# Kernel tuning notes

Measured on AMD Instinct MI355X. Metric: run time of the kernel, lower is better.

## Reference

```python
import jax, jax.numpy as jnp
import numpy as np

B, C, HID, H, W = 32, 256, 128, 32, 32  # batch, input_dim, hidden_dim, grid


def conv1x1(x, Wt, b):
    # 1x1 Conv2d == channel-mixing matmul. x: [B,Cin,H,W], Wt: [Cout,Cin]
    return jnp.einsum('oc,bchw->bohw', Wt, x) + b[None, :, None, None]


def setup_inputs() -> dict:
    key = jax.random.key(0)
    ks = jax.random.split(key, 18)
    p = lambda k, shape: (jax.random.normal(k, shape, jnp.float32) * 0.02)
    return {
        'h': jax.random.normal(ks[0], (B, C, H, W), jnp.float32),
        'm': jax.random.normal(ks[1], (B, C, H, W), jnp.float32),
        'Wq': p(ks[2], (HID, C)),  'bq': p(ks[3], (HID,)),
        'Wk': p(ks[4], (HID, C)),  'bk': p(ks[5], (HID,)),
        'Wv': p(ks[6], (C, C)),    'bv': p(ks[7], (C,)),
        'Wk2': p(ks[8], (HID, C)), 'bk2': p(ks[9], (HID,)),
        'Wv2': p(ks[10], (C, C)),  'bv2': p(ks[11], (C,)),
        'Wz': p(ks[12], (2 * C, 2 * C)), 'bz': p(ks[13], (2 * C,)),
        'Wm': p(ks[14], (3 * C, 3 * C)), 'bm': p(ks[15], (3 * C,)),
    }


def reference(h, m, Wq, bq, Wk, bk, Wv, bv, Wk2, bk2, Wv2, bv2, Wz, bz, Wm, bm):
    Bb, Cc, Hh, Ww = h.shape
    HW = Hh * Ww
    # shared query from h: [B, HID, HW]
    q = conv1x1(h, Wq, bq).reshape(Bb, -1, HW)
    # self-attention branch over h (unscaled logits, as in original)
    kh = conv1x1(h, Wk, bk).reshape(Bb, -1, HW)
    A_h = jax.nn.softmax(jnp.einsum('bdp,bdq->bpq', q, kh), axis=-1)  # [B,HW,HW]
    vh = conv1x1(h, Wv, bv).reshape(Bb, Cc, HW)
    Z_h = jnp.einsum('bpq,bcq->bcp', A_h, vh).reshape(Bb, Cc, Hh, Ww)
    # cross-attention branch over memory m with shared q
    km = conv1x1(m, Wk2, bk2).reshape(Bb, -1, HW)
    A_m = jax.nn.softmax(jnp.einsum('bdp,bdq->bpq', q, km), axis=-1)
    vm = conv1x1(m, Wv2, bv2).reshape(Bb, Cc, HW)
    Z_m = jnp.einsum('bpq,bcq->bcp', A_m, vm).reshape(Bb, Cc, Hh, Ww)
    # fuse, then LSTM-style gating
    Z = conv1x1(jnp.concatenate([Z_h, Z_m], axis=1), Wz, bz)          # [B,2C,H,W]
    comb = conv1x1(jnp.concatenate([Z, h], axis=1), Wm, bm)           # [B,3C,H,W]
    mo, mg, mi = jnp.split(comb, 3, axis=1)
    mi = jax.nn.sigmoid(mi)
    new_m = (1.0 - mi) * m + mi * jnp.tanh(mg)
    new_h = jax.nn.sigmoid(mo) * new_m
    return new_h, new_m
```

## Files before the change

### kernel.cpp

```cpp
#include <hip/hip_runtime.h>
#include <hip/hip_bf16.h>

typedef __bf16  v8bf __attribute__((ext_vector_type(8)));
typedef float   v4f  __attribute__((ext_vector_type(4)));
typedef float   f4   __attribute__((ext_vector_type(4)));
typedef unsigned short us8 __attribute__((ext_vector_type(8)));
typedef unsigned short us4 __attribute__((ext_vector_type(4)));
typedef unsigned int u32;

#define BATCH 32
#define CDIM  256
#define HW    1024

#define OFF_HBT 0L
#define OFF_MBT (OFF_HBT + 16777216L)
#define OFF_QKH (OFF_MBT + 16777216L)
#define OFF_QKM (OFF_QKH + 16777216L)
#define OFF_VH  (OFF_QKM + 8388608L)
#define OFF_VM  (OFF_VH  + 16777216L)
#define OFF_ZCT (OFF_VM  + 16777216L)
#define OFF_W   (OFF_ZCT + 33554432L)
#define OFF_B   (OFF_W   + 3866624L)
#define WS_TOTAL (OFF_B + 2944L * 4)
#define W_QK  0
#define W_K2  65536
#define W_V   98304
#define W_V2  163840
#define W_M   491520
#define W_ZT  1081344
#define W_F   1343488
#define B_QK  0
#define B_K2  256
#define B_V   384
#define B_V2  640
#define B_F   2176

__device__ inline unsigned short f2u(float x) {
    __hip_bfloat16 h = __float2bfloat16(x);
    union { __hip_bfloat16 h; unsigned short u; } cv; cv.h = h; return cv.u;
}
__device__ inline float u2f(unsigned short u) {
    union { unsigned short u; __hip_bfloat16 h; } cv; cv.u = u; return __bfloat162float(cv.h);
}
__device__ inline float sigmoidf_(float x) {
    x = fminf(fmaxf(x, -30.f), 30.f);
    return 1.f / (1.f + __expf(-x));
}
__device__ inline float tanhf_(float x) {
    x = fminf(fmaxf(x, -15.f), 15.f);
    float e = __expf(2.f * x);
    return (e - 1.f) / (e + 1.f);
}
__device__ inline void glds16(const unsigned short* g, unsigned short* l) {
    __builtin_amdgcn_global_load_lds(
        (const __attribute__((address_space(1))) u32*)g,
        (__attribute__((address_space(3))) u32*)l, 16, 0, 0);
}

__global__ __launch_bounds__(256)
void prep(const float* __restrict__ hsrc, const float* __restrict__ msrc,
          const float* __restrict__ Wq, const float* __restrict__ Wk,
          const float* __restrict__ Wv, const float* __restrict__ Wk2,
          const float* __restrict__ Wv2, const float* __restrict__ Wz,
          const float* __restrict__ Wm,
          const float* __restrict__ bq, const float* __restrict__ bk,
          const float* __restrict__ bk2, const float* __restrict__ bv,
          const float* __restrict__ bv2, const float* __restrict__ bz,
          const float* __restrict__ bm,
          char* __restrict__ ws)
{
    __shared__ float t[64][68];
    unsigned short* wdst = (unsigned short*)(ws + OFF_W);
    float*          bdst = (float*)(ws + OFF_B);
    const int bid = blockIdx.x;
    const int tid = threadIdx.x;

    if (bid < 6025) {
        const int gid = bid * 256 + tid;
        if (gid < 1081344) {
            const float* s; int off;
            if      (gid <   32768) { s = Wq;  off = gid; }
            else if (gid <   65536) { s = Wk;  off = gid -   32768; }
            else if (gid <   98304) { s = Wk2; off = gid -   65536; }
            else if (gid <  163840) { s = Wv;  off = gid -   98304; }
            else if (gid <  229376) { s = Wv2; off = gid -  163840; }
            else if (gid <  491520) { s = Wz;  off = gid -  229376; }
            else                    { s = Wm;  off = gid -  491520; }
            wdst[gid] = f2u(s[off]);
        } else if (gid < 1343488) {
            const int idx = gid - 1081344;
            const int k = idx >> 9, j = idx & 511;
            wdst[gid] = f2u(Wz[j * 512 + k]);
        } else if (gid < 1540096) {
            const int idx = gid - 1343488;
            const int o = idx >> 8, kk = 512 + (idx & 255);
            wdst[W_F + o * 768 + kk] = f2u(Wm[o * 768 + kk]);
        } else {
            const int bi = gid - 1540096;
            if (bi < 2176) {
                const float* s; int off;
                if      (bi <  128) { s = bq;  off = bi; }
                else if (bi <  256) { s = bk;  off = bi -  128; }
                else if (bi <  384) { s = bk2; off = bi -  256; }
                else if (bi <  640) { s = bv;  off = bi -  384; }
                else if (bi <  896) { s = bv2; off = bi -  640; }
                else if (bi < 1408) { s = bz;  off = bi -  896; }
                else                { s = bm;  off = bi - 1408; }
                bdst[bi] = s[off];
            }
        }
    } else if (bid < 6028) {
        const int o = (bid - 6025) * 256 + tid;
        if (o < 768) {
            float s = bm[o];
            const float* r = Wm + (long)o * 768;
#pragma unroll 8
            for (int j = 0; j < 512; ++j) s += r[j] * bz[j];
            bdst[B_F + o] = s;
        }
    } else {
        const int tz = bid - 6028;
        const int z  = tz >> 6;
        const int p0 = (tz & 15) * 64;
        const int c0 = ((tz >> 4) & 3) * 64;
        const float* src = (z < BATCH) ? hsrc + (long)z * CDIM * HW
                                       : msrc + (long)(z - BATCH) * CDIM * HW;
        unsigned short* dst = (unsigned short*)(ws + ((z < BATCH) ? OFF_HBT : OFF_MBT))
                              + (long)((z < BATCH) ? z : z - BATCH) * HW * CDIM;
        const int r  = tid >> 4;
        const int c4 = (tid & 15) * 4;
#pragma unroll
        for (int i = 0; i < 4; ++i) {
            const f4 v = *reinterpret_cast<const f4*>(src + (long)(c0 + r + 16 * i) * HW + p0 + c4);
            t[r + 16 * i][c4 + 0] = v[0];
            t[r + 16 * i][c4 + 1] = v[1];
            t[r + 16 * i][c4 + 2] = v[2];
            t[r + 16 * i][c4 + 3] = v[3];
        }
        __syncthreads();
#pragma unroll
        for (int i = 0; i < 4; ++i) {
            const int pr = r + 16 * i;
            us4 o;
#pragma unroll
            for (int j = 0; j < 4; ++j) o[j] = f2u(t[c4 + j][pr]);
            *reinterpret_cast<us4*>(dst + (long)(p0 + pr) * CDIM + c0 + c4) = o;
        }
    }
}

__device__ __forceinline__
void gemm_core(const unsigned short* __restrict__ A, int lda,
               const unsigned short* __restrict__ A2, int lda2, int kswitch,
               const unsigned short* __restrict__ Bt, int ldb,
               unsigned short* __restrict__ Cp, int ldc,
               int K, const float* __restrict__ bias, int biasMode,
               int m0, int n0,
               unsigned short* As, unsigned short* Bs)
{
    const int tid  = threadIdx.x;
    const int lane = tid & 63;
    const int w    = tid >> 6;

    v4f acc[4][4];
#pragma unroll
    for (int i = 0; i < 4; ++i)
#pragma unroll
        for (int j = 0; j < 4; ++j) acc[i][j] = v4f{0.f, 0.f, 0.f, 0.f};

    const int wm   = (w >> 1) * 64;
    const int wn   = (w & 1) * 64;
    const int fr   = lane & 15;
    const int g    = lane >> 4;

    const int arow = (w << 3) + (lane >> 3);
    const int acol = (((lane & 7) ^ ((lane >> 3) & 7)) * 8);
    const int lbase = (w << 9);

    for (int k0 = 0; k0 < K; k0 += 64) {
        const unsigned short* Ab; int Al; int Ao;
        if (k0 < kswitch) { Ab = A;  Al = lda;  Ao = k0; }
        else              { Ab = A2; Al = lda2; Ao = k0 - kswitch; }
        const unsigned short* ga = Ab + (long)(m0 + arow) * Al + Ao + acol;
        const unsigned short* gb = Bt + (long)(n0 + arow) * ldb + k0 + acol;
#pragma unroll
        for (int i = 0; i < 4; ++i) {
            glds16(ga + (long)(32 * i) * Al, &As[i * 2048 + lbase]);
            glds16(gb + (long)(32 * i) * ldb, &Bs[i * 2048 + lbase]);
        }
        __syncthreads();
#pragma unroll
        for (int ks = 0; ks < 2; ++ks) {
            const int slot = ((ks * 4 + g) ^ (fr & 7)) * 8;
            v8bf af[4], bfv[4];
#pragma unroll
            for (int mi = 0; mi < 4; ++mi)
                af[mi] = *reinterpret_cast<const v8bf*>(&As[(wm + mi * 16 + fr) * 64 + slot]);
#pragma unroll
            for (int ni = 0; ni < 4; ++ni)
                bfv[ni] = *reinterpret_cast<const v8bf*>(&Bs[(wn + ni * 16 + fr) * 64 + slot]);
#pragma unroll
            for (int mi = 0; mi < 4; ++mi)
#pragma unroll
                for (int ni = 0; ni < 4; ++ni)
                    acc[mi][ni] = __builtin_amdgcn_mfma_f32_16x16x32_bf16(af[mi], bfv[ni], acc[mi][ni], 0, 0, 0);
        }
        __syncthreads();
    }

    const int rbase0 = m0 + wm + g * 4;
#pragma unroll
    for (int mi = 0; mi < 4; ++mi) {
#pragma unroll
        for (int ni = 0; ni < 4; ++ni) {
            const int col = n0 + wn + ni * 16 + fr;
            const int rb  = rbase0 + mi * 16;
            const float bn = (biasMode == 1) ? bias[col] : 0.f;
#pragma unroll
            for (int r = 0; r < 4; ++r) {
                float x = acc[mi][ni][r] + bn;
                if (biasMode == 2) x += bias[rb + r];
                Cp[(long)(rb + r) * ldc + col] = f2u(x);
            }
        }
    }
}

__global__ __launch_bounds__(256)
void gemm_multi(char* __restrict__ ws)
{
    __shared__ unsigned short As[128 * 64];
    __shared__ unsigned short Bs[128 * 64];
    unsigned short* wA = (unsigned short*)(ws + OFF_W);
    float*          bA = (float*)(ws + OFF_B);
    const int id = blockIdx.x;

    if (id < 512) {
        const int b = id >> 4, x = id & 7, y = (id >> 3) & 1;
        const unsigned short* A = (unsigned short*)(ws + OFF_HBT) + (long)b * 262144;
        gemm_core(A, 256, A, 256, 1 << 30, wA + W_QK, 256,
                  (unsigned short*)(ws + OFF_QKH) + (long)b * 262144, 256,
                  256, bA + B_QK, 1, x * 128, y * 128, As, Bs);
    } else if (id < 768) {
        const int idx = id - 512, b = idx >> 3, x = idx & 7;
        const unsigned short* A = (unsigned short*)(ws + OFF_MBT) + (long)b * 262144;
        gemm_core(A, 256, A, 256, 1 << 30, wA + W_K2, 256,
                  (unsigned short*)(ws + OFF_QKM) + (long)b * 131072, 128,
                  256, bA + B_K2, 1, x * 128, 0, As, Bs);
    } else if (id < 1280) {
        const int idx = id - 768, b = idx >> 4, x = idx & 1, y = (idx >> 1) & 7;
        gemm_core(wA + W_V, 256, wA + W_V, 256, 1 << 30,
                  (unsigned short*)(ws + OFF_HBT) + (long)b * 262144, 256,
                  (unsigned short*)(ws + OFF_VH) + (long)b * 262144, 1024,
                  256, bA + B_V, 2, x * 128, y * 128, As, Bs);
    } else if (id < 1792) {
        const int idx = id - 1280, b = idx >> 4, x = idx & 1, y = (idx >> 1) & 7;
        gemm_core(wA + W_V2, 256, wA + W_V2, 256, 1 << 30,
                  (unsigned short*)(ws + OFF_MBT) + (long)b * 262144, 256,
                  (unsigned short*)(ws + OFF_VM) + (long)b * 262144, 1024,
                  256, bA + B_V2, 2, x * 128, y * 128, As, Bs);
    } else {
        const int idx = id - 1792, x = idx % 6, y = idx / 6;
        gemm_core(wA + W_M, 768, wA + W_M, 768, 1 << 30, wA + W_ZT, 512,
                  wA + W_F, 768, 512, bA, 0, x * 128, y * 128, As, Bs);
    }
}

__global__ __launch_bounds__(512, 2)
void comb_gemm(const unsigned short* __restrict__ A, int lda,
               const unsigned short* __restrict__ A2, int lda2, int kswitch,
               const unsigned short* __restrict__ Bt, int ldb,
               int K, const float* __restrict__ bias,
               const float* __restrict__ mIn,
               float* __restrict__ outh, float* __restrict__ outm)
{
    __shared__ unsigned short smem[57344];

    const int nwg = gridDim.x;
    const int wg  = (blockIdx.x & 7) * (nwg >> 3) + (blockIdx.x >> 3);
    const int m0  = (wg >> 2) * 256;
    const int c0  = (wg & 3) * 64;

    const int tid  = threadIdx.x;
    const int lane = tid & 63;
    const int w    = tid >> 6;
    const int fr   = lane & 15;
    const int g    = lane >> 4;
    const int wm   = (w >> 2) * 128;
    const int wn   = (w & 3) * 48;

    const int srow   = tid >> 3;
    const int schunk = ((tid & 7) ^ (srow & 7)) * 8;
    const int sdst   = w * 512;

    v4f acc[8][3];
#pragma unroll
    for (int i = 0; i < 8; ++i)
#pragma unroll
        for (int j = 0; j < 3; ++j) acc[i][j] = v4f{0.f, 0.f, 0.f, 0.f};

    const int nt = K >> 6;

#define STAGE_A(t, bi, i)                                                      \
    { const int k0 = (t) * 64;                                                 \
      const unsigned short* Ab; int Al; int Ao;                                \
      if (k0 < kswitch) { Ab = A;  Al = lda;  Ao = k0; }                       \
      else              { Ab = A2; Al = lda2; Ao = k0 - kswitch; }             \
      glds16(Ab + (long)(m0 + (i) * 64 + srow) * Al + Ao + schunk,             \
             &smem[(bi) * 16384 + (i) * 4096 + sdst]); }
#define STAGE_B(t, bi, i)                                                      \
    { const int k0 = (t) * 64;                                                 \
      glds16(Bt + (long)((i) * 256 + c0 + srow) * ldb + k0 + schunk,           \
             &smem[32768 + (bi) * 12288 + (i) * 4096 + sdst]); }

#pragma unroll
    for (int i = 0; i < 4; ++i) STAGE_A(0, 0, i);
#pragma unroll
    for (int i = 0; i < 3; ++i) STAGE_B(0, 0, i);

    for (int t = 0; t < nt; ++t) {
        __syncthreads();

        const unsigned short* Ar = smem + (t & 1) * 16384;
        const unsigned short* Br = smem + 32768 + (t & 1) * 12288;
        const int nb = (t + 1) & 1;
        const bool more = (t + 1 < nt);

#pragma unroll
        for (int ks = 0; ks < 2; ++ks) {
            v8bf bf[3];
#pragma unroll
            for (int ni = 0; ni < 3; ++ni) {
                const int r = wn + ni * 16 + fr;
                bf[ni] = *reinterpret_cast<const v8bf*>(
                    &Br[r * 64 + ((ks * 4 + g) ^ (r & 7)) * 8]);
            }
#pragma unroll
            for (int hh = 0; hh < 2; ++hh) {
                v8bf af[4];
#pragma unroll
                for (int mi = 0; mi < 4; ++mi) {
                    const int r = wm + (hh * 4 + mi) * 16 + fr;
                    af[mi] = *reinterpret_cast<const v8bf*>(
                        &Ar[r * 64 + ((ks * 4 + g) ^ (r & 7)) * 8]);
                }
                if (more) {
                    const int ph = ks * 2 + hh;
                    if (ph == 0)      { STAGE_A(t + 1, nb, 0); STAGE_A(t + 1, nb, 1); }
                    else if (ph == 1) { STAGE_A(t + 1, nb, 2); STAGE_A(t + 1, nb, 3); }
                    else if (ph == 2) { STAGE_B(t + 1, nb, 0); STAGE_B(t + 1, nb, 1); }
                    else              { STAGE_B(t + 1, nb, 2); }
                }
                __builtin_amdgcn_s_setprio(1);
#pragma unroll
                for (int mi = 0; mi < 4; ++mi)
#pragma unroll
                    for (int ni = 0; ni < 3; ++ni)
                        acc[hh * 4 + mi][ni] = __builtin_amdgcn_mfma_f32_16x16x32_bf16(
                            af[mi], bf[ni], acc[hh * 4 + mi][ni], 0, 0, 0);
                __builtin_amdgcn_s_setprio(0);
            }
        }
    }
#undef STAGE_A
#undef STAGE_B

    __syncthreads();

    unsigned short* Lt = smem;
#pragma unroll
    for (int mi = 0; mi < 8; ++mi) {
#pragma unroll
        for (int ni = 0; ni < 3; ++ni) {
            const int j  = wn + ni * 16 + fr;
            const int cg = ((j >> 6) << 8) + c0 + (j & 63);
            const float bn = bias[cg];
            const int rl = wm + mi * 16 + g * 4;
#pragma unroll
            for (int r = 0; r < 4; ++r)
                Lt[(rl + r) * 194 + j] = f2u(acc[mi][ni][r] + bn);
        }
    }
    __syncthreads();

    const int b     = m0 >> 10;
    const int pbase = m0 & 1023;
    const int pl    = tid & 255;
    const int ch    = tid >> 8;
#pragma unroll 4
    for (int cc = 0; cc < 32; ++cc) {
        const int cl = ch * 32 + cc;
        const float mo  = u2f(Lt[pl * 194 + cl]);
        const float mg  = u2f(Lt[pl * 194 + 64 + cl]);
        const float mi_ = u2f(Lt[pl * 194 + 128 + cl]);
        const long gi = ((long)(b * 256 + c0 + cl)) * 1024 + pbase + pl;
        const float mv = mIn[gi];
        const float ms = sigmoidf_(mi_);
        const float nm = (1.f - ms) * mv + ms * tanhf_(mg);
        const float nh = sigmoidf_(mo) * nm;
        outh[gi] = nh;
        outm[gi] = nm;
    }
}

__global__ __launch_bounds__(512, 4)
void attn_fused(const unsigned short* __restrict__ Qb, long sQ, int ldq,
                const unsigned short* __restrict__ K0, long sK0, int ldk0,
                const unsigned short* __restrict__ V0,
                const unsigned short* __restrict__ K1, long sK1, int ldk1,
                const unsigned short* __restrict__ V1,
                unsigned short* __restrict__ Out, long sO)
{
    __shared__ unsigned short Qs[64 * 128];
    __shared__ unsigned short Ks[64 * 128];
    __shared__ unsigned short Vs[256 * 64];
    __shared__ unsigned short Ps[64 * 64];

    const int id = blockIdx.x;
    const int c8 = id & 7;
    const int k  = id >> 3;
    const int z  = c8 * 8 + (k >> 4);
    const int p0 = (k & 15) * 64;

    const int b  = (z < 32) ? z : z - 32;
    const unsigned short* Kp; const unsigned short* Vp; int ldk, outoff;
    if (z < 32) { Kp = K0 + (long)b * sK0; Vp = V0 + (long)b * 262144L; ldk = ldk0; outoff = 0; }
    else        { Kp = K1 + (long)b * sK1; Vp = V1 + (long)b * 262144L; ldk = ldk1; outoff = 256; }
    const unsigned short* Qp = Qb + (long)b * sQ;
    Out += (long)b * sO;

    const int tid  = threadIdx.x;
    const int lane = tid & 63;
    const int w    = tid >> 6;
    const int fr   = lane & 15;
    const int g    = lane >> 4;
    const int wp   = w >> 2;
    const int wq   = w & 3;

    v4f vacc[2][4];
#pragma unroll
    for (int i = 0; i < 2; ++i)
#pragma unroll
        for (int j = 0; j < 4; ++j) vacc[i][j] = v4f{0.f, 0.f, 0.f, 0.f};
    float rp[2][4];
#pragma unroll
    for (int i = 0; i < 2; ++i)
#pragma unroll
        for (int r = 0; r < 4; ++r) rp[i][r] = 0.f;

    const int srow   = tid >> 4;
    const int schunk = ((tid & 15) ^ (srow & 7)) * 8;
    const int vrow   = tid >> 3;
    const int vchunk = ((tid & 7) ^ (vrow & 7)) * 8;
    const int sdst   = w * 512;
    const int kr     = wq * 16 + fr;

#define STAGE_Q()                                                              \
    { _Pragma("unroll")                                                        \
      for (int i = 0; i < 2; ++i)                                              \
          glds16(Qp + (long)(p0 + i * 32 + srow) * ldq + schunk,               \
                 &Qs[i * 4096 + sdst]); }
#define STAGE_K(t)                                                             \
    { const int kv0 = (t) * 64;                                                \
      _Pragma("unroll")                                                        \
      for (int i = 0; i < 2; ++i)                                              \
          glds16(Kp + (long)(kv0 + i * 32 + srow) * ldk + schunk,              \
                 &Ks[i * 4096 + sdst]); }
#define STAGE_V(t)                                                             \
    { const int kv0 = (t) * 64;                                                \
      _Pragma("unroll")                                                        \
      for (int i = 0; i < 4; ++i)                                              \
          glds16(Vp + (long)(i * 64 + vrow) * 1024 + kv0 + vchunk,             \
                 &Vs[i * 4096 + sdst]); }

    STAGE_Q();
    STAGE_K(0);

    for (int t = 0; t < 16; ++t) {
        __syncthreads();
        STAGE_V(t);

        v4f sacc[2];
#pragma unroll
        for (int mi = 0; mi < 2; ++mi) sacc[mi] = v4f{0.f, 0.f, 0.f, 0.f};
        __builtin_amdgcn_s_setprio(1);
#pragma unroll
        for (int ks = 0; ks < 4; ++ks) {
            const v8bf kf = *reinterpret_cast<const v8bf*>(
                &Ks[kr * 128 + ((ks * 4 + g) ^ (kr & 7)) * 8]);
#pragma unroll
            for (int mi = 0; mi < 2; ++mi) {
                const int qrow = wp * 32 + mi * 16 + fr;
                const v8bf qf = *reinterpret_cast<const v8bf*>(
                    &Qs[qrow * 128 + ((ks * 4 + g) ^ (qrow & 7)) * 8]);
                sacc[mi] = __builtin_amdgcn_mfma_f32_16x16x32_bf16(qf, kf, sacc[mi], 0, 0, 0);
            }
        }
        __builtin_amdgcn_s_setprio(0);
#pragma unroll
        for (int mi = 0; mi < 2; ++mi)
#pragma unroll
            for (int r = 0; r < 4; ++r) {
                const float e = __expf(sacc[mi][r]);
                rp[mi][r] += e;
                const int prow = wp * 32 + mi * 16 + g * 4 + r;
                Ps[prow * 64 + (kr ^ ((prow & 7) << 3))] = f2u(e);
            }

        __syncthreads();
        if (t < 15) STAGE_K(t + 1);

        __builtin_amdgcn_s_setprio(1);
#pragma unroll
        for (int ks = 0; ks < 2; ++ks) {
            v8bf pf[2], vf[4];
#pragma unroll
            for (int mi = 0; mi < 2; ++mi) {
                const int pr = wp * 32 + mi * 16 + fr;
                pf[mi] = *reinterpret_cast<const v8bf*>(
                    &Ps[pr * 64 + ((ks * 4 + g) ^ (pr & 7)) * 8]);
            }
#pragma unroll
            for (int ni = 0; ni < 4; ++ni) {
                const int vr = wq * 64 + ni * 16 + fr;
                vf[ni] = *reinterpret_cast<const v8bf*>(
                    &Vs[vr * 64 + ((ks * 4 + g) ^ (vr & 7)) * 8]);
            }
#pragma unroll
            for (int mi = 0; mi < 2; ++mi)
#pragma unroll
                for (int ni = 0; ni < 4; ++ni)
                    vacc[mi][ni] = __builtin_amdgcn_mfma_f32_16x16x32_bf16(pf[mi], vf[ni], vacc[mi][ni], 0, 0, 0);
        }
        __builtin_amdgcn_s_setprio(0);
    }
#undef STAGE_Q
#undef STAGE_K
#undef STAGE_V

    __syncthreads();
    float* red = reinterpret_cast<float*>(Ps);
#pragma unroll
    for (int mi = 0; mi < 2; ++mi)
#pragma unroll
        for (int r = 0; r < 4; ++r) {
            float v = rp[mi][r];
            v += __shfl_xor(v, 1);
            v += __shfl_xor(v, 2);
            v += __shfl_xor(v, 4);
            v += __shfl_xor(v, 8);
            if (fr == 0) red[wq * 64 + wp * 32 + mi * 16 + g * 4 + r] = v;
        }
    __syncthreads();

#pragma unroll
    for (int mi = 0; mi < 2; ++mi)
#pragma unroll
        for (int r = 0; r < 4; ++r) {
            const int pl = wp * 32 + mi * 16 + g * 4 + r;
            const float inv = 1.f / (red[pl] + red[64 + pl] + red[128 + pl] + red[192 + pl]);
#pragma unroll
            for (int ni = 0; ni < 4; ++ni)
                Out[(long)(p0 + pl) * 512 + outoff + wq * 64 + ni * 16 + fr]
                    = f2u(vacc[mi][ni][r] * inv);
        }
}

extern "C" void kernel_launch(void* const* d_in, const int* in_sizes, int n_in,
                              void* d_out, int out_size, void* d_ws, size_t ws_size,
                              hipStream_t stream)
{
    const float* h   = (const float*)d_in[0];
    const float* m   = (const float*)d_in[1];
    const float* Wq  = (const float*)d_in[2];
    const float* bq  = (const float*)d_in[3];
    const float* Wk  = (const float*)d_in[4];
    const float* bk  = (const float*)d_in[5];
    const float* Wv  = (const float*)d_in[6];
    const float* bv  = (const float*)d_in[7];
    const float* Wk2 = (const float*)d_in[8];
    const float* bk2 = (const float*)d_in[9];
    const float* Wv2 = (const float*)d_in[10];
    const float* bv2 = (const float*)d_in[11];
    const float* Wz  = (const float*)d_in[12];
    const float* bz  = (const float*)d_in[13];
    const float* Wm  = (const float*)d_in[14];
    const float* bm  = (const float*)d_in[15];

    char* ws = (char*)d_ws;
    if (ws_size < (size_t)WS_TOTAL) return;

    unsigned short* hT  = (unsigned short*)(ws + OFF_HBT);
    unsigned short* qkh = (unsigned short*)(ws + OFF_QKH);
    unsigned short* qkm = (unsigned short*)(ws + OFF_QKM);
    unsigned short* vh  = (unsigned short*)(ws + OFF_VH);
    unsigned short* vm  = (unsigned short*)(ws + OFF_VM);
    unsigned short* zct = (unsigned short*)(ws + OFF_ZCT);
    unsigned short* wA  = (unsigned short*)(ws + OFF_W);
    float*          bA  = (float*)(ws + OFF_B);

    float* outh = (float*)d_out;
    float* outm = outh + 8388608L;

    prep<<<dim3(10124), dim3(256), 0, stream>>>(
        h, m, Wq, Wk, Wv, Wk2, Wv2, Wz, Wm,
        bq, bk, bk2, bv, bv2, bz, bm, ws);

    gemm_multi<<<dim3(1816), dim3(256), 0, stream>>>(ws);

    attn_fused<<<dim3(1024), dim3(512), 0, stream>>>(
        qkh, 262144L, 256,
        qkh + 128, 262144L, 256, vh,
        qkm, 131072L, 128, vm,
        zct, 524288L);

    comb_gemm<<<dim3(512), dim3(512), 0, stream>>>(
        zct, 512, hT, 256, 512,
        wA + W_F, 768, 768, bA + B_F, m, outh, outm);
}
```

Baseline: 205.4 us.

## Retile attention to 128 query rows per block with 32-wide KV steps

The fused attention kernel now gives each block 128 query rows instead of 64, so each block covers a full PV output tile per wave (4x4 MFMA accumulators). K/V tiles shrink to 32 keys per iteration, with twice as many iterations. The aim is to halve re-reading of K and V across blocks and raise MFMA work per LDS load. The cost is more accumulator registers, more barriers per unit of work, and only 512 blocks, which may hurt occupancy and load balance.

```diff
diff --git a/kernel.cpp b/kernel.cpp
--- a/kernel.cpp
+++ b/kernel.cpp
@@ -411,16 +411,16 @@
                 const unsigned short* __restrict__ V1,
                 unsigned short* __restrict__ Out, long sO)
 {
-    __shared__ unsigned short Qs[64 * 128];
-    __shared__ unsigned short Ks[64 * 128];
-    __shared__ unsigned short Vs[256 * 64];
-    __shared__ unsigned short Ps[64 * 64];
+    __shared__ unsigned short Qs[128 * 128];
+    __shared__ unsigned short Ks[32 * 128];
+    __shared__ unsigned short Vs[256 * 32];
+    __shared__ unsigned short Ps[128 * 32];
 
     const int id = blockIdx.x;
     const int c8 = id & 7;
     const int k  = id >> 3;
-    const int z  = c8 * 8 + (k >> 4);
-    const int p0 = (k & 15) * 64;
+    const int z  = c8 * 8 + (k >> 3);
+    const int p0 = (k & 7) * 128;
 
     const int b  = (z < 32) ? z : z - 32;
     const unsigned short* Kp; const unsigned short* Vp; int ldk, outoff;
@@ -436,10 +436,14 @@
     const int g    = lane >> 4;
     const int wp   = w >> 2;
     const int wq   = w & 3;
-
-    v4f vacc[2][4];
-#pragma unroll
-    for (int i = 0; i < 2; ++i)
+    const int srow0 = wp * 64 + (wq >> 1) * 32;
+    const int kc0   = (wq & 1) * 16;
+    const int kr    = kc0 + fr;
+    const int wc    = wq * 64;
+
+    v4f vacc[4][4];
+#pragma unroll
+    for (int i = 0; i < 4; ++i)
 #pragma unroll
         for (int j = 0; j < 4; ++j) vacc[i][j] = v4f{0.f, 0.f, 0.f, 0.f};
     float rp[2][4];
@@ -448,35 +452,30 @@
 #pragma unroll
         for (int r = 0; r < 4; ++r) rp[i][r] = 0.f;
 
-    const int srow   = tid >> 4;
-    const int schunk = ((tid & 15) ^ (srow & 7)) * 8;
-    const int vrow   = tid >> 3;
-    const int vchunk = ((tid & 7) ^ (vrow & 7)) * 8;
+    const int qkrow  = tid >> 4;
+    const int qkchk  = ((tid & 15) ^ (qkrow & 7)) * 8;
+    const int vrow   = tid >> 2;
+    const int vchk   = ((tid & 3) ^ (vrow & 3)) * 8;
     const int sdst   = w * 512;
-    const int kr     = wq * 16 + fr;
 
 #define STAGE_Q()                                                              \
     { _Pragma("unroll")                                                        \
-      for (int i = 0; i < 2; ++i)                                              \
-          glds16(Qp + (long)(p0 + i * 32 + srow) * ldq + schunk,               \
+      for (int i = 0; i < 4; ++i)                                              \
+          glds16(Qp + (long)(p0 + i * 32 + qkrow) * ldq + qkchk,               \
                  &Qs[i * 4096 + sdst]); }
 #define STAGE_K(t)                                                             \
-    { const int kv0 = (t) * 64;                                                \
+    glds16(Kp + (long)((t) * 32 + qkrow) * ldk + qkchk, &Ks[sdst]);
+#define STAGE_V(t)                                                             \
+    { const int kv0 = (t) * 32;                                                \
       _Pragma("unroll")                                                        \
       for (int i = 0; i < 2; ++i)                                              \
-          glds16(Kp + (long)(kv0 + i * 32 + srow) * ldk + schunk,              \
-                 &Ks[i * 4096 + sdst]); }
-#define STAGE_V(t)                                                             \
-    { const int kv0 = (t) * 64;                                                \
-      _Pragma("unroll")                                                        \
-      for (int i = 0; i < 4; ++i)                                              \
-          glds16(Vp + (long)(i * 64 + vrow) * 1024 + kv0 + vchunk,             \
+          glds16(Vp + (long)(i * 128 + vrow) * 1024 + kv0 + vchk,              \
                  &Vs[i * 4096 + sdst]); }
 
     STAGE_Q();
     STAGE_K(0);
 
-    for (int t = 0; t < 16; ++t) {
+    for (int t = 0; t < 32; ++t) {
         __syncthreads();
         STAGE_V(t);
 
@@ -490,7 +489,7 @@
                 &Ks[kr * 128 + ((ks * 4 + g) ^ (kr & 7)) * 8]);
 #pragma unroll
             for (int mi = 0; mi < 2; ++mi) {
-                const int qrow = wp * 32 + mi * 16 + fr;
+                const int qrow = srow0 + mi * 16 + fr;
                 const v8bf qf = *reinterpret_cast<const v8bf*>(
                     &Qs[qrow * 128 + ((ks * 4 + g) ^ (qrow & 7)) * 8]);
                 sacc[mi] = __builtin_amdgcn_mfma_f32_16x16x32_bf16(qf, kf, sacc[mi], 0, 0, 0);
@@ -503,31 +502,30 @@
             for (int r = 0; r < 4; ++r) {
                 const float e = __expf(sacc[mi][r]);
                 rp[mi][r] += e;
-                const int prow = wp * 32 + mi * 16 + g * 4 + r;
-                Ps[prow * 64 + (kr ^ ((prow & 7) << 3))] = f2u(e);
+                const int prow = srow0 + mi * 16 + g * 4 + r;
+                Ps[prow * 32 + (((kr >> 3) ^ (prow & 3)) << 3) + (kr & 7)] = f2u(e);
             }
 
         __syncthreads();
-        if (t < 15) STAGE_K(t + 1);
+        if (t < 31) STAGE_K(t + 1);
 
         __builtin_amdgcn_s_setprio(1);
-#pragma unroll
-        for (int ks = 0; ks < 2; ++ks) {
-            v8bf pf[2], vf[4];
-#pragma unroll
-            for (int mi = 0; mi < 2; ++mi) {
-                const int pr = wp * 32 + mi * 16 + fr;
+        {
+            v8bf pf[4], vf[4];
+#pragma unroll
+            for (int mi = 0; mi < 4; ++mi) {
+                const int pr = wp * 64 + mi * 16 + fr;
                 pf[mi] = *reinterpret_cast<const v8bf*>(
-                    &Ps[pr * 64 + ((ks * 4 + g) ^ (pr & 7)) * 8]);
+                    &Ps[pr * 32 + ((g ^ (pr & 3)) << 3)]);
             }
 #pragma unroll
             for (int ni = 0; ni < 4; ++ni) {
-                const int vr = wq * 64 + ni * 16 + fr;
+                const int vr = wc + ni * 16 + fr;
                 vf[ni] = *reinterpret_cast<const v8bf*>(
-                    &Vs[vr * 64 + ((ks * 4 + g) ^ (vr & 7)) * 8]);
-            }
-#pragma unroll
-            for (int mi = 0; mi < 2; ++mi)
+                    &Vs[vr * 32 + ((g ^ (vr & 3)) << 3)]);
+            }
+#pragma unroll
+            for (int mi = 0; mi < 4; ++mi)
 #pragma unroll
                 for (int ni = 0; ni < 4; ++ni)
                     vacc[mi][ni] = __builtin_amdgcn_mfma_f32_16x16x32_bf16(pf[mi], vf[ni], vacc[mi][ni], 0, 0, 0);
@@ -549,19 +547,19 @@
             v += __shfl_xor(v, 2);
             v += __shfl_xor(v, 4);
             v += __shfl_xor(v, 8);
-            if (fr == 0) red[wq * 64 + wp * 32 + mi * 16 + g * 4 + r] = v;
+            if (fr == 0) red[(wq & 1) * 128 + srow0 + mi * 16 + g * 4 + r] = v;
         }
     __syncthreads();
 
 #pragma unroll
-    for (int mi = 0; mi < 2; ++mi)
+    for (int mi = 0; mi < 4; ++mi)
 #pragma unroll
         for (int r = 0; r < 4; ++r) {
-            const int pl = wp * 32 + mi * 16 + g * 4 + r;
-            const float inv = 1.f / (red[pl] + red[64 + pl] + red[128 + pl] + red[192 + pl]);
+            const int pl = wp * 64 + mi * 16 + g * 4 + r;
+            const float inv = 1.f / (red[pl] + red[128 + pl]);
 #pragma unroll
             for (int ni = 0; ni < 4; ++ni)
-                Out[(long)(p0 + pl) * 512 + outoff + wq * 64 + ni * 16 + fr]
+                Out[(long)(p0 + pl) * 512 + outoff + wc + ni * 16 + fr]
                     = f2u(vacc[mi][ni][r] * inv);
         }
 }
@@ -608,7 +606,7 @@
 
     gemm_multi<<<dim3(1816), dim3(256), 0, stream>>>(ws);
 
-    attn_fused<<<dim3(1024), dim3(512), 0, stream>>>(
+    attn_fused<<<dim3(512), dim3(512), 0, stream>>>(
         qkh, 262144L, 256,
         qkh + 128, 262144L, 256, vh,
         qkm, 131072L, 128, vm,
```

Result: no change. 201.7 us (-1.8%).
